# Kernel optimization log

Measured on AMD Instinct MI355X. Metric: run time of the kernel, lower is better.

The kernel has to match this reference:

```python
import jax, jax.numpy as jnp
import numpy as np

SLOPE = 5.0                # surrogate gradient slope (SurrogateGradient default)
REFRACTORY_PERIOD = 2.0    # config.refractory_period
ADAPT_DECAY = 0.9          # threshold_adapt EMA decay
ADAPT_INC = 0.1


@jax.custom_vjp
def spike_fn(membrane, threshold):
    # Heaviside spike with surrogate gradient (fast sigmoid), matching SurrogateGradient
    return (membrane >= threshold).astype(membrane.dtype)

def _spike_fwd(membrane, threshold):
    return spike_fn(membrane, threshold), (membrane, threshold)

def _spike_bwd(res, g):
    membrane, threshold = res
    s = jax.nn.sigmoid(SLOPE * (membrane - threshold))
    grad_m = g * SLOPE * s * (1.0 - s)
    # torch returns None (zero) grad for threshold through the spike op itself
    return grad_m, jnp.zeros_like(threshold)

spike_fn.defvjp(_spike_fwd, _spike_bwd)


def setup_inputs() -> dict:
    key = jax.random.key(0)
    kx, = jax.random.split(key, 1)
    B, S, D = 16, 2048, 1024
    x = jax.random.normal(kx, (B, S, D), dtype=jnp.float32)
    beta_mem = jnp.asarray(0.9, dtype=jnp.float32)                      # membrane_decay
    beta_syn = jnp.exp(jnp.asarray(-1.0 / 5.0, dtype=jnp.float32))      # exp(-1/tau_syn)
    threshold_adapt_p = jnp.full((1,), 0.1, dtype=jnp.float32)          # nn.Parameter ones(1)*0.1
    threshold_scale = jnp.ones((D,), dtype=jnp.float32)
    learnable_threshold = jnp.ones((D,), dtype=jnp.float32)             # threshold=1.0
    return {
        "x": x,
        "beta_mem": beta_mem,
        "beta_syn": beta_syn,
        "threshold_adapt_p": threshold_adapt_p,
        "threshold_scale": threshold_scale,
        "learnable_threshold": learnable_threshold,
    }


def _lif(x, beta_mem, beta_syn, threshold_adapt_p, threshold_scale, learnable_threshold):
    B, S, D = x.shape
    z = jnp.zeros((B, D), dtype=x.dtype)
    init = (z, z, z, z)  # membrane, synaptic, threshold_adapt, refractory

    def step(carry, xt):  # xt: (B, D)
        membrane, synaptic, th_adapt, refractory = carry
        synaptic = beta_syn * synaptic + xt
        non_refractory = (refractory <= 0).astype(x.dtype)
        membrane = beta_mem * membrane + synaptic * non_refractory
        cur_th = learnable_threshold + threshold_adapt_p * th_adapt * threshold_scale
        spikes = spike_fn(membrane, cur_th)
        membrane = membrane - spikes * cur_th  # reset_mode='subtract'
        th_adapt = ADAPT_DECAY * th_adapt + ADAPT_INC * spikes
        refractory = jnp.where(
            spikes > 0.5,
            jnp.full_like(spikes, REFRACTORY_PERIOD),
            jnp.clip(refractory - 1.0, 0.0),
        )
        return (membrane, synaptic, th_adapt, refractory), spikes

    carry, spikes = jax.lax.scan(step, init, jnp.swapaxes(x, 0, 1))  # scan over seq
    spike_train = jnp.swapaxes(spikes, 0, 1)  # (B, S, D)
    return spike_train, carry


def reference(x, beta_mem, beta_syn, threshold_adapt_p, threshold_scale, learnable_threshold):
    spike_train, (membrane, synaptic, th_adapt, refractory) = _lif(
        x, beta_mem, beta_syn, threshold_adapt_p, threshold_scale, learnable_threshold
    )
    return spike_train, membrane, synaptic, th_adapt, refractory
```

## Files before the change

### kernel.cpp

```cpp
#include <hip/hip_runtime.h>
#include <stdint.h>


#define SB 16
#define SS 2048
#define SD 1024
#define TILE 64
#define NT (SS / TILE)

typedef const __attribute__((address_space(1))) void* gas_ptr;
typedef __attribute__((address_space(3))) void* las_ptr;

__global__ __launch_bounds__(128, 1) void lif_kernel(
    const float* __restrict__ x,
    const float* __restrict__ beta_mem_p,
    const float* __restrict__ beta_syn_p,
    const float* __restrict__ adapt_p,
    const float* __restrict__ scale_p,
    const float* __restrict__ lth_p,
    float* __restrict__ out)
{
#pragma clang fp contract(off)
    __shared__ __attribute__((aligned(16))) float xbuf[3][TILE][64];
    __shared__ float sbuf[2][64][TILE + 1];

    const int bk = blockIdx.x;
    const int b  = bk >> 4;
    const int d0 = (bk & 15) << 6;

    if (threadIdx.x < 64) {
        const int lane = threadIdx.x;
        const int d    = d0 + lane;

        const float beta_mem = beta_mem_p[0];
        const float beta_syn = beta_syn_p[0];
        const float p        = adapt_p[0];
        const float scale    = scale_p[d];
        const float lth      = lth_p[d];

        float mem = 0.f, syn = 0.f, tha = 0.f;
        bool  nref = true;
        bool  f1 = false, f2 = false;

        __syncthreads();

        int cbuf = 0;
        for (int k = 0; k < NT; ++k) {
            const int sb = k & 1;

            float xa[16], xbv[16], xc[16], xd[16];
            #pragma unroll
            for (int i = 0; i < 16; ++i) xa[i]  = xbuf[cbuf][i][lane];
            #pragma unroll
            for (int i = 0; i < 16; ++i) xbv[i] = xbuf[cbuf][16 + i][lane];
            #pragma unroll
            for (int i = 0; i < 16; ++i) xc[i]  = xbuf[cbuf][32 + i][lane];
            #pragma unroll
            for (int i = 0; i < 16; ++i) xd[i]  = xbuf[cbuf][48 + i][lane];

            auto step = [&](float xt, int ti) {
                syn = __builtin_fmaf(beta_syn, syn, xt);
                const float syn_eff = nref ? syn : 0.f;
                const float memf = __builtin_fmaf(beta_mem, mem, syn_eff);
                const float q      = p * tha;
                const float cur_th = __builtin_fmaf(q, scale, lth);
                const bool  fired  = (memf >= cur_th);
                const float spike  = fired ? 1.f : 0.f;
                mem = __builtin_fmaf(-spike, cur_th, memf);
                tha = __builtin_fmaf(0.9f, tha, 0.1f * spike);
                nref = !(fired || f1);
                f2 = f1; f1 = fired;
                sbuf[sb][lane][ti] = spike;
            };

            #pragma unroll
            for (int i = 0; i < 16; ++i) step(xa[i], i);
            #pragma unroll
            for (int i = 0; i < 16; ++i) step(xbv[i], 16 + i);
            #pragma unroll
            for (int i = 0; i < 16; ++i) step(xc[i], 32 + i);
            #pragma unroll
            for (int i = 0; i < 16; ++i) step(xd[i], 48 + i);

            __syncthreads();
            cbuf = (cbuf == 2) ? 0 : cbuf + 1;
        }

        const float refr = f1 ? 2.0f : (f2 ? 1.0f : 0.0f);
        const size_t base = (size_t)SB * SS * SD;
        const size_t off  = (size_t)b * SD + d;
        out[base + 0 * (size_t)SB * SD + off] = mem;
        out[base + 1 * (size_t)SB * SD + off] = syn;
        out[base + 2 * (size_t)SB * SD + off] = tha;
        out[base + 3 * (size_t)SB * SD + off] = refr;
    } else {
        const int hl = threadIdx.x - 64;

        const float* xb   = x   + ((size_t)b * SS) * SD + d0;
        float*       outb = out + ((size_t)b * SS) * SD + d0;

        const int srow = hl >> 4;
        const int scol = (hl & 15) << 2;
        const float* src_base = xb + (size_t)srow * SD + scol;

        auto issue_tile = [&](int k, int buf) {
            const float* s0 = src_base + (size_t)(k * TILE) * SD;
            float* dst = &xbuf[buf][0][0];
            #pragma unroll
            for (int r = 0; r < 16; ++r) {
                __builtin_amdgcn_global_load_lds(
                    (gas_ptr)(s0 + (size_t)(r * 4) * SD),
                    (las_ptr)(dst + r * 4 * 64),
                    16, 0, 0);
            }
        };

        auto store_tile = [&](int tk) {
            const int sb = tk & 1;
            int idx = tk * TILE * SD + hl;
            #pragma unroll 8
            for (int t = 0; t < TILE; ++t) {
                outb[idx] = sbuf[sb][hl][t];
                idx += SD;
            }
        };

        issue_tile(0, 0);
        issue_tile(1, 1);
        __syncthreads();

        int nbuf = 2;
        for (int k = 0; k < NT; ++k) {
            if (k + 2 < NT) {
                issue_tile(k + 2, nbuf);
                nbuf = (nbuf == 2) ? 0 : nbuf + 1;
            }
            if (k >= 1) store_tile(k - 1);
            __syncthreads();
        }
        store_tile(NT - 1);
    }
}

extern "C" void kernel_launch(void* const* d_in, const int* in_sizes, int n_in,
                              void* d_out, int out_size, void* d_ws, size_t ws_size,
                              hipStream_t stream) {
    const float* x        = (const float*)d_in[0];
    const float* beta_mem = (const float*)d_in[1];
    const float* beta_syn = (const float*)d_in[2];
    const float* adapt_p  = (const float*)d_in[3];
    const float* scale    = (const float*)d_in[4];
    const float* lth      = (const float*)d_in[5];
    float* out = (float*)d_out;

    lif_kernel<<<256, 128, 0, stream>>>(x, beta_mem, beta_syn, adapt_p, scale, lth, out);
}
```

Measured before the change: 77.64 us.

## Offload synaptic recurrence to producer wave via shared synbuf staging

The producer wave now computes the synaptic-current recurrence for each tile and writes it into a new double-buffered shared array, one tile ahead of the compute wave. The compute wave reads precomputed synaptic values, so its serial per-step dependency chain drops one FMA. Input staging goes from triple to double buffering to make room for the new buffer. The producer wave takes on extra LDS traffic and arithmetic between its loads and stores, which could make it the new bottleneck.

```diff
diff --git a/kernel.cpp b/kernel.cpp
--- a/kernel.cpp
+++ b/kernel.cpp
@@ -21,7 +21,8 @@
     float* __restrict__ out)
 {
 #pragma clang fp contract(off)
-    __shared__ __attribute__((aligned(16))) float xbuf[3][TILE][64];
+    __shared__ __attribute__((aligned(16))) float xbuf[2][TILE][64];
+    __shared__ __attribute__((aligned(16))) float synbuf[2][TILE][64];
     __shared__ float sbuf[2][64][TILE + 1];
 
     const int bk = blockIdx.x;
@@ -33,34 +34,32 @@
         const int d    = d0 + lane;
 
         const float beta_mem = beta_mem_p[0];
-        const float beta_syn = beta_syn_p[0];
         const float p        = adapt_p[0];
         const float scale    = scale_p[d];
         const float lth      = lth_p[d];
 
-        float mem = 0.f, syn = 0.f, tha = 0.f;
+        float mem = 0.f, tha = 0.f;
         bool  nref = true;
         bool  f1 = false, f2 = false;
 
         __syncthreads();
+        __syncthreads();
 
-        int cbuf = 0;
         for (int k = 0; k < NT; ++k) {
             const int sb = k & 1;
 
-            float xa[16], xbv[16], xc[16], xd[16];
+            float sa[16], sbv[16], sc[16], sd_[16];
             #pragma unroll
-            for (int i = 0; i < 16; ++i) xa[i]  = xbuf[cbuf][i][lane];
+            for (int i = 0; i < 16; ++i) sa[i]  = synbuf[sb][i][lane];
             #pragma unroll
-            for (int i = 0; i < 16; ++i) xbv[i] = xbuf[cbuf][16 + i][lane];
+            for (int i = 0; i < 16; ++i) sbv[i] = synbuf[sb][16 + i][lane];
             #pragma unroll
-            for (int i = 0; i < 16; ++i) xc[i]  = xbuf[cbuf][32 + i][lane];
+            for (int i = 0; i < 16; ++i) sc[i]  = synbuf[sb][32 + i][lane];
             #pragma unroll
-            for (int i = 0; i < 16; ++i) xd[i]  = xbuf[cbuf][48 + i][lane];
+            for (int i = 0; i < 16; ++i) sd_[i] = synbuf[sb][48 + i][lane];
 
-            auto step = [&](float xt, int ti) {
-                syn = __builtin_fmaf(beta_syn, syn, xt);
-                const float syn_eff = nref ? syn : 0.f;
+            auto step = [&](float sv, int ti) {
+                const float syn_eff = nref ? sv : 0.f;
                 const float memf = __builtin_fmaf(beta_mem, mem, syn_eff);
                 const float q      = p * tha;
                 const float cur_th = __builtin_fmaf(q, scale, lth);
@@ -74,28 +73,27 @@
             };
 
             #pragma unroll
-            for (int i = 0; i < 16; ++i) step(xa[i], i);
+            for (int i = 0; i < 16; ++i) step(sa[i], i);
             #pragma unroll
-            for (int i = 0; i < 16; ++i) step(xbv[i], 16 + i);
+            for (int i = 0; i < 16; ++i) step(sbv[i], 16 + i);
             #pragma unroll
-            for (int i = 0; i < 16; ++i) step(xc[i], 32 + i);
+            for (int i = 0; i < 16; ++i) step(sc[i], 32 + i);
             #pragma unroll
-            for (int i = 0; i < 16; ++i) step(xd[i], 48 + i);
+            for (int i = 0; i < 16; ++i) step(sd_[i], 48 + i);
 
             __syncthreads();
-            cbuf = (cbuf == 2) ? 0 : cbuf + 1;
         }
 
         const float refr = f1 ? 2.0f : (f2 ? 1.0f : 0.0f);
         const size_t base = (size_t)SB * SS * SD;
         const size_t off  = (size_t)b * SD + d;
         out[base + 0 * (size_t)SB * SD + off] = mem;
-        out[base + 1 * (size_t)SB * SD + off] = syn;
         out[base + 2 * (size_t)SB * SD + off] = tha;
         out[base + 3 * (size_t)SB * SD + off] = refr;
     } else {
         const int hl = threadIdx.x - 64;
 
+        const float beta_syn = beta_syn_p[0];
         const float* xb   = x   + ((size_t)b * SS) * SD + d0;
         float*       outb = out + ((size_t)b * SS) * SD + d0;
 
@@ -115,6 +113,22 @@
             }
         };
 
+        float hsyn = 0.f;
+        auto syn_tile = [&](int k) {
+            const int xs = k & 1;
+            #pragma unroll
+            for (int g = 0; g < 4; ++g) {
+                float xv[16];
+                #pragma unroll
+                for (int i = 0; i < 16; ++i) xv[i] = xbuf[xs][g * 16 + i][hl];
+                #pragma unroll
+                for (int i = 0; i < 16; ++i) {
+                    hsyn = __builtin_fmaf(beta_syn, hsyn, xv[i]);
+                    synbuf[xs][g * 16 + i][hl] = hsyn;
+                }
+            }
+        };
+
         auto store_tile = [&](int tk) {
             const int sb = tk & 1;
             int idx = tk * TILE * SD + hl;
@@ -128,17 +142,19 @@
         issue_tile(0, 0);
         issue_tile(1, 1);
         __syncthreads();
+        syn_tile(0);
+        __syncthreads();
 
-        int nbuf = 2;
         for (int k = 0; k < NT; ++k) {
-            if (k + 2 < NT) {
-                issue_tile(k + 2, nbuf);
-                nbuf = (nbuf == 2) ? 0 : nbuf + 1;
-            }
+            if (k + 1 < NT) syn_tile(k + 1);
+            if (k + 2 < NT) issue_tile(k + 2, k & 1);
             if (k >= 1) store_tile(k - 1);
             __syncthreads();
         }
         store_tile(NT - 1);
+
+        const size_t base = (size_t)SB * SS * SD;
+        out[base + 1 * (size_t)SB * SD + (size_t)b * SD + d0 + hl] = hsyn;
     }
 }
 
```

New measurement: 76.92 us. No clear change (-0.9%).
